# Kernel tuning notes

Hardware: AMD Instinct MI355X
Metric: run time of the kernel (lower is better)

The kernel has to match this reference:

```python
import jax, jax.numpy as jnp
import numpy as np

D_HEAD = 128
H_Q = 16
H_K = 4
D_MODEL = 2048
B = 2
T = 2048


def setup_inputs() -> dict:
    key = jax.random.key(0)
    k1, k2, k3, k4, k5 = jax.random.split(key, 5)
    s = 0.02
    return {
        "x": jax.random.normal(k1, (B, T, D_MODEL), dtype=jnp.float32),
        "wq": jax.random.normal(k2, (D_HEAD * H_Q, D_MODEL), dtype=jnp.float32) * s,
        "wk": jax.random.normal(k3, (D_HEAD * H_K, D_MODEL), dtype=jnp.float32) * s,
        "wv": jax.random.normal(k4, (D_HEAD * H_K, D_MODEL), dtype=jnp.float32) * s,
        "wo": jax.random.normal(k5, (D_MODEL, D_HEAD * H_Q), dtype=jnp.float32) * s,
    }


def reference(x, wq, wk, wv, wo):
    Bs, Ts, _ = x.shape
    g = H_Q // H_K  # query groups per kv head
    # projections (torch Linear: y = x @ W^T)
    Q = (x @ wq.T).reshape(Bs, Ts, H_Q, D_HEAD).transpose(0, 2, 1, 3)  # [B,hq,T,d]
    K = (x @ wk.T).reshape(Bs, Ts, H_K, D_HEAD).transpose(0, 2, 1, 3)  # [B,hk,T,d]
    V = (x @ wv.T).reshape(Bs, Ts, H_K, D_HEAD).transpose(0, 2, 1, 3)  # [B,hk,T,d]
    Qg = Q.reshape(Bs, g, H_K, Ts, D_HEAD)  # [B,g,hk,T,d]
    scale = D_HEAD ** -0.5
    attn = jnp.einsum("bghtd,bhsd->bghts", Qg, K) * scale  # [B,g,hk,T,T]
    causal = jnp.tril(jnp.ones((Ts, Ts), dtype=bool))
    attn = jnp.where(causal, attn, -jnp.inf)
    attn = jax.nn.softmax(attn, axis=-1)
    out = jnp.einsum("bghts,bhsd->bghtd", attn, V)  # [B,g,hk,T,d]
    out = out.reshape(Bs, H_Q, Ts, D_HEAD).transpose(0, 2, 1, 3).reshape(Bs, Ts, H_Q * D_HEAD)
    return out @ wo.T
```

## Files before the change

kernel.cpp:

```cpp
#include <hip/hip_runtime.h>
#include <hip/hip_bf16.h>
#include <stdint.h>

#define DMODEL 2048
#define HQ 16
#define HKV 4
#define DH 128
#define SEQT 2048
#define BATCH 2

typedef __bf16 bf16x8 __attribute__((ext_vector_type(8)));
typedef float f32x4 __attribute__((ext_vector_type(4)));
typedef float f32x16 __attribute__((ext_vector_type(16)));
typedef unsigned short u16x4 __attribute__((ext_vector_type(4)));
typedef unsigned short u16x8 __attribute__((ext_vector_type(8)));
typedef unsigned int u32x2 __attribute__((ext_vector_type(2)));

__device__ __forceinline__ unsigned short f2bf(float x) {
  __hip_bfloat16 h = __float2bfloat16(x);
  return __builtin_bit_cast(unsigned short, h);
}
__device__ __forceinline__ unsigned int cvtpk(float a, float b) {
  unsigned int r;
  asm("v_cvt_pk_bf16_f32 %0, %1, %2" : "=v"(r) : "v"(a), "v"(b));
  return r;
}

__device__ __forceinline__ void gload_lds16(const void* g, void* lds) {
  __builtin_amdgcn_global_load_lds(
      (const __attribute__((address_space(1))) void*)(uintptr_t)g,
      (__attribute__((address_space(3))) void*)(uint32_t)(uintptr_t)lds,
      16, 0, 0);
}

__global__ __launch_bounds__(256) void cast_all_kernel(
    const float* __restrict__ x, const float* __restrict__ wq,
    const float* __restrict__ wk, const float* __restrict__ wv,
    const float* __restrict__ wo,
    unsigned short* __restrict__ xb, unsigned short* __restrict__ wqb,
    unsigned short* __restrict__ wkb, unsigned short* __restrict__ wvb,
    unsigned short* __restrict__ wob) {
  int i = blockIdx.x * 256 + threadIdx.x;
  const float* in; unsigned short* out; int off; float s = 1.0f;
  if (i < 1048576)      { in = x;  out = xb;  off = i; }
  else if (i < 1572864) { in = wq; out = wqb; off = i - 1048576; s = 0.1275174473f; }
  else if (i < 1703936) { in = wk; out = wkb; off = i - 1572864; }
  else if (i < 1835008) { in = wv; out = wvb; off = i - 1703936; }
  else                  { in = wo; out = wob; off = i - 1835008; }
  const float4* p = reinterpret_cast<const float4*>(in) + (size_t)off * 2;
  float4 a = p[0], b = p[1];
  u16x8 o;
  o[0] = f2bf(a.x * s); o[1] = f2bf(a.y * s); o[2] = f2bf(a.z * s); o[3] = f2bf(a.w * s);
  o[4] = f2bf(b.x * s); o[5] = f2bf(b.y * s); o[6] = f2bf(b.z * s); o[7] = f2bf(b.w * s);
  *(reinterpret_cast<u16x8*>(out) + off) = o;
}

template <bool OUT_BF16>
__device__ __forceinline__ void gemm_body(
    unsigned short* As, unsigned short* Bs,
    const unsigned short* __restrict__ A, const unsigned short* __restrict__ B,
    void* __restrict__ Cv, int N, int K, int row0, int col0) {
  const int tid = threadIdx.x;
  const int wave = tid >> 6, lane = tid & 63;
  const int wr = (wave >> 1) * 64, wc = (wave & 1) * 64;
  const int l15 = lane & 15, l4 = lane >> 4;
  const int srow = wave * 32 + (lane >> 2);
  const int scol = (lane & 3) * 8;

  f32x4 acc[4][4] = {};

  for (int k0 = 0; k0 < K; k0 += 64) {
#pragma unroll
    for (int h = 0; h < 2; ++h) {
      const unsigned short* gA = A + (size_t)(row0 + srow) * K + k0 + h * 32 + scol;
      gload_lds16(gA, (char*)As + h * 8192 + wave * 2048);
      gload_lds16(gA + (size_t)16 * K, (char*)As + h * 8192 + wave * 2048 + 1024);
      const unsigned short* gB = B + (size_t)(col0 + srow) * K + k0 + h * 32 + scol;
      gload_lds16(gB, (char*)Bs + h * 8192 + wave * 2048);
      gload_lds16(gB + (size_t)16 * K, (char*)Bs + h * 8192 + wave * 2048 + 1024);
    }
    __syncthreads();

    bf16x8 af[2][4], bfr[2][4];
#pragma unroll
    for (int h = 0; h < 2; ++h)
#pragma unroll
      for (int i = 0; i < 4; ++i) {
        af[h][i]  = *reinterpret_cast<const bf16x8*>(&As[h * 4096 + (wr + i * 16 + l15) * 32 + l4 * 8]);
        bfr[h][i] = *reinterpret_cast<const bf16x8*>(&Bs[h * 4096 + (wc + i * 16 + l15) * 32 + l4 * 8]);
      }
#pragma unroll
    for (int h = 0; h < 2; ++h)
#pragma unroll
      for (int i = 0; i < 4; ++i)
#pragma unroll
        for (int j = 0; j < 4; ++j)
          acc[i][j] = __builtin_amdgcn_mfma_f32_16x16x32_bf16(af[h][i], bfr[h][j], acc[i][j], 0, 0, 0);
    __syncthreads();
  }

#pragma unroll
  for (int i = 0; i < 4; ++i) {
    const int rrow = row0 + wr + i * 16 + l4 * 4;
#pragma unroll
    for (int j = 0; j < 4; ++j) {
      const int ccol = col0 + wc + j * 16 + l15;
#pragma unroll
      for (int r = 0; r < 4; ++r) {
        const size_t idx = (size_t)(rrow + r) * N + ccol;
        if constexpr (OUT_BF16)
          ((unsigned short*)Cv)[idx] = f2bf(acc[i][j][r]);
        else
          ((float*)Cv)[idx] = acc[i][j][r];
      }
    }
  }
}

__global__ __launch_bounds__(256) void gemm_qkv(
    const unsigned short* __restrict__ xb, const unsigned short* __restrict__ wqb,
    const unsigned short* __restrict__ wkb, const unsigned short* __restrict__ wvb,
    unsigned short* __restrict__ Qb, unsigned short* __restrict__ Kb,
    unsigned short* __restrict__ VTb) {
  __shared__ alignas(16) unsigned short As[2][128 * 32];
  __shared__ alignas(16) unsigned short Bs[2][128 * 32];
  const int bid = blockIdx.x;
  if (bid < 512) {
    gemm_body<true>(&As[0][0], &Bs[0][0], xb, wqb, Qb, 2048, DMODEL,
                    (bid >> 4) * 128, (bid & 15) * 128);
  } else if (bid < 640) {
    const int r = bid - 512;
    gemm_body<true>(&As[0][0], &Bs[0][0], xb, wkb, Kb, 512, DMODEL,
                    (r >> 2) * 128, (r & 3) * 128);
  } else {
    const int r = bid - 640;
    const int tz = r & 1, ty = (r >> 1) & 15, tx = r >> 5;
    gemm_body<true>(&As[0][0], &Bs[0][0], wvb,
                    xb + (size_t)tz * SEQT * DMODEL,
                    VTb + (size_t)tz * 512 * SEQT, SEQT, DMODEL,
                    tx * 128, ty * 128);
  }
}

template <bool OUT_BF16>
__global__ __launch_bounds__(256) void gemm_bt(
    const unsigned short* __restrict__ A, const unsigned short* __restrict__ B,
    void* __restrict__ Cv, int N, int K) {
  __shared__ alignas(16) unsigned short As[2][128 * 32];
  __shared__ alignas(16) unsigned short Bs[2][128 * 32];
  gemm_body<OUT_BF16>(&As[0][0], &Bs[0][0], A, B, Cv, N, K,
                      blockIdx.x * 128, blockIdx.y * 128);
}

__global__ __launch_bounds__(256, 2) void attn_kernel(
    const unsigned short* __restrict__ Q, const unsigned short* __restrict__ Kc,
    const unsigned short* __restrict__ VT, unsigned short* __restrict__ AO) {
  __shared__ alignas(16) unsigned short Ks[2][16 * 512];
  __shared__ alignas(16) unsigned short Vs[2][16 * 512];

  const int tid = threadIdx.x;
  const int wave = tid >> 6, lane = tid & 63;
  const int bid = blockIdx.x;
  const int round = bid >> 8, pairslot = bid & 255;
  const int bhk = pairslot & 7;
  const int jp = pairslot >> 3;
  const int j = round ? jp : 63 - jp;
  const int b = bhk >> 2, hk = bhk & 3;
  const int h = hk + wave * 4;
  const int q0 = j * 32;
  const int jt = j >> 1;
  const int lq = lane & 31, hi = lane >> 5;

  const size_t qrow = (size_t)(b * SEQT + q0 + lq);
  const unsigned short* qp = Q + qrow * (HQ * DH) + h * DH + hi * 8;
  bf16x8 qf[8];
#pragma unroll
  for (int dc = 0; dc < 8; ++dc)
    qf[dc] = *reinterpret_cast<const bf16x8*>(qp + dc * 16);

  f32x16 acc[4] = {};
  float mrun = -INFINITY, lrun = 0.f;

  const unsigned short* kbase = Kc + (size_t)b * SEQT * (HKV * DH) + hk * DH;
  const unsigned short* vtb = VT + ((size_t)b * (HKV * DH) + hk * DH) * SEQT;

  auto STAGE = [&](int buf, int kvb2) {
#pragma unroll
    for (int i = 0; i < 4; ++i) {
      const int f = i * 4 + wave;
      const int sub = f >> 3, dc = f & 7;
      const unsigned short* g = kbase + (size_t)(kvb2 + sub * 32 + lq) * (HKV * DH) + dc * 16 + hi * 8;
      gload_lds16(g, (char*)Ks[buf] + f * 1024);
    }
#pragma unroll
    for (int i = 0; i < 4; ++i) {
      const int f = i * 4 + wave;
      const int dt = f >> 2, ks = f & 3;
      const unsigned short* g = vtb + (size_t)(dt * 32 + lq) * SEQT + kvb2 + ks * 16 + hi * 8;
      gload_lds16(g, (char*)Vs[buf] + f * 1024);
    }
  };

  STAGE(0, 0);
  __syncthreads();
  int cur = 0;

  for (int t = 0; t <= jt; ++t) {
    const int kvb = t * 64;
    if (t < jt) STAGE(cur ^ 1, kvb + 64);
    const bool s1v = (kvb + 32 <= q0);
    const bool d0 = (kvb == q0), d1 = (kvb + 32 == q0);
    const char* ksb = (const char*)Ks[cur];
    const char* vsb = (const char*)Vs[cur];

    f32x16 stA = {}, stB = {}, stA1 = {}, stB1 = {};
    __builtin_amdgcn_s_setprio(1);
#pragma unroll
    for (int dc = 0; dc < 4; ++dc) {
      bf16x8 kf = *reinterpret_cast<const bf16x8*>(ksb + dc * 1024 + lane * 16);
      stA = __builtin_amdgcn_mfma_f32_32x32x16_bf16(kf, qf[dc], stA, 0, 0, 0);
    }
#pragma unroll
    for (int dc = 4; dc < 8; ++dc) {
      bf16x8 kf = *reinterpret_cast<const bf16x8*>(ksb + dc * 1024 + lane * 16);
      stB = __builtin_amdgcn_mfma_f32_32x32x16_bf16(kf, qf[dc], stB, 0, 0, 0);
    }
    if (s1v) {
#pragma unroll
      for (int dc = 0; dc < 4; ++dc) {
        bf16x8 kf = *reinterpret_cast<const bf16x8*>(ksb + (8 + dc) * 1024 + lane * 16);
        stA1 = __builtin_amdgcn_mfma_f32_32x32x16_bf16(kf, qf[dc], stA1, 0, 0, 0);
      }
#pragma unroll
      for (int dc = 4; dc < 8; ++dc) {
        bf16x8 kf = *reinterpret_cast<const bf16x8*>(ksb + (8 + dc) * 1024 + lane * 16);
        stB1 = __builtin_amdgcn_mfma_f32_32x32x16_bf16(kf, qf[dc], stB1, 0, 0, 0);
      }
    }
    __builtin_amdgcn_s_setprio(0);

    float p0[16], p1[16];
#pragma unroll
    for (int r = 0; r < 16; ++r) p0[r] = stA[r] + stB[r];
    if (d0) {
#pragma unroll
      for (int r = 0; r < 16; ++r) {
        const int srw = (r & 3) + 8 * (r >> 2) + 4 * hi;
        if (srw > lq) p0[r] = -INFINITY;
      }
    }
    float m0, m1 = -INFINITY;
    {
      float a = fmaxf(fmaxf(p0[0], p0[1]), fmaxf(p0[2], p0[3]));
      float bm = fmaxf(fmaxf(p0[4], p0[5]), fmaxf(p0[6], p0[7]));
      float c = fmaxf(fmaxf(p0[8], p0[9]), fmaxf(p0[10], p0[11]));
      float dm = fmaxf(fmaxf(p0[12], p0[13]), fmaxf(p0[14], p0[15]));
      m0 = fmaxf(fmaxf(a, bm), fmaxf(c, dm));
    }
    if (s1v) {
#pragma unroll
      for (int r = 0; r < 16; ++r) p1[r] = stA1[r] + stB1[r];
      if (d1) {
#pragma unroll
        for (int r = 0; r < 16; ++r) {
          const int srw = (r & 3) + 8 * (r >> 2) + 4 * hi;
          if (srw > lq) p1[r] = -INFINITY;
        }
      }
      float a = fmaxf(fmaxf(p1[0], p1[1]), fmaxf(p1[2], p1[3]));
      float bm = fmaxf(fmaxf(p1[4], p1[5]), fmaxf(p1[6], p1[7]));
      float c = fmaxf(fmaxf(p1[8], p1[9]), fmaxf(p1[10], p1[11]));
      float dm = fmaxf(fmaxf(p1[12], p1[13]), fmaxf(p1[14], p1[15]));
      m1 = fmaxf(fmaxf(a, bm), fmaxf(c, dm));
    }
    float tmax = fmaxf(m0, m1);
    tmax = fmaxf(tmax, __shfl_xor(tmax, 32));
    if (!__all(tmax <= mrun)) {
      const float mnew = fmaxf(mrun, tmax);
      const float fsc = __builtin_amdgcn_exp2f(mrun - mnew);
      lrun *= fsc;
#pragma unroll
      for (int dt = 0; dt < 4; ++dt)
#pragma unroll
        for (int r = 0; r < 16; ++r) acc[dt][r] *= fsc;
      mrun = mnew;
    }
    float psum;
    {
#pragma unroll
      for (int r = 0; r < 16; ++r) p0[r] = __builtin_amdgcn_exp2f(p0[r] - mrun);
      float t0 = (p0[0] + p0[1]) + (p0[2] + p0[3]);
      float t1 = (p0[4] + p0[5]) + (p0[6] + p0[7]);
      float t2 = (p0[8] + p0[9]) + (p0[10] + p0[11]);
      float t3 = (p0[12] + p0[13]) + (p0[14] + p0[15]);
      psum = (t0 + t1) + (t2 + t3);
    }
    if (s1v) {
#pragma unroll
      for (int r = 0; r < 16; ++r) p1[r] = __builtin_amdgcn_exp2f(p1[r] - mrun);
      float t0 = (p1[0] + p1[1]) + (p1[2] + p1[3]);
      float t1 = (p1[4] + p1[5]) + (p1[6] + p1[7]);
      float t2 = (p1[8] + p1[9]) + (p1[10] + p1[11]);
      float t3 = (p1[12] + p1[13]) + (p1[14] + p1[15]);
      psum += (t0 + t1) + (t2 + t3);
    }

    union { unsigned int u[4]; bf16x8 v; } pf0, pf1, pf2, pf3;
    {
      unsigned int x0 = cvtpk(p0[0], p0[1]),  x1 = cvtpk(p0[2], p0[3]);
      unsigned int x2 = cvtpk(p0[4], p0[5]),  x3 = cvtpk(p0[6], p0[7]);
      unsigned int x4 = cvtpk(p0[8], p0[9]),  x5 = cvtpk(p0[10], p0[11]);
      unsigned int x6 = cvtpk(p0[12], p0[13]), x7 = cvtpk(p0[14], p0[15]);
      unsigned int x0s = __shfl_xor(x0, 32), x1s = __shfl_xor(x1, 32);
      unsigned int x2s = __shfl_xor(x2, 32), x3s = __shfl_xor(x3, 32);
      unsigned int x4s = __shfl_xor(x4, 32), x5s = __shfl_xor(x5, 32);
      unsigned int x6s = __shfl_xor(x6, 32), x7s = __shfl_xor(x7, 32);
      pf0.u[0] = hi ? x2s : x0;  pf0.u[1] = hi ? x3s : x1;
      pf0.u[2] = hi ? x2  : x0s; pf0.u[3] = hi ? x3  : x1s;
      pf1.u[0] = hi ? x6s : x4;  pf1.u[1] = hi ? x7s : x5;
      pf1.u[2] = hi ? x6  : x4s; pf1.u[3] = hi ? x7  : x5s;
    }
    if (s1v) {
      unsigned int x0 = cvtpk(p1[0], p1[1]),  x1 = cvtpk(p1[2], p1[3]);
      unsigned int x2 = cvtpk(p1[4], p1[5]),  x3 = cvtpk(p1[6], p1[7]);
      unsigned int x4 = cvtpk(p1[8], p1[9]),  x5 = cvtpk(p1[10], p1[11]);
      unsigned int x6 = cvtpk(p1[12], p1[13]), x7 = cvtpk(p1[14], p1[15]);
      unsigned int x0s = __shfl_xor(x0, 32), x1s = __shfl_xor(x1, 32);
      unsigned int x2s = __shfl_xor(x2, 32), x3s = __shfl_xor(x3, 32);
      unsigned int x4s = __shfl_xor(x4, 32), x5s = __shfl_xor(x5, 32);
      unsigned int x6s = __shfl_xor(x6, 32), x7s = __shfl_xor(x7, 32);
      pf2.u[0] = hi ? x2s : x0;  pf2.u[1] = hi ? x3s : x1;
      pf2.u[2] = hi ? x2  : x0s; pf2.u[3] = hi ? x3  : x1s;
      pf3.u[0] = hi ? x6s : x4;  pf3.u[1] = hi ? x7s : x5;
      pf3.u[2] = hi ? x6  : x4s; pf3.u[3] = hi ? x7  : x5s;
    }
    psum += __shfl_xor(psum, 32);
    lrun += psum;

    __builtin_amdgcn_s_setprio(1);
#pragma unroll
    for (int dt = 0; dt < 4; ++dt) {
      bf16x8 v0 = *reinterpret_cast<const bf16x8*>(vsb + (dt * 4 + 0) * 1024 + lane * 16);
      bf16x8 v1 = *reinterpret_cast<const bf16x8*>(vsb + (dt * 4 + 1) * 1024 + lane * 16);
      acc[dt] = __builtin_amdgcn_mfma_f32_32x32x16_bf16(v0, pf0.v, acc[dt], 0, 0, 0);
      acc[dt] = __builtin_amdgcn_mfma_f32_32x32x16_bf16(v1, pf1.v, acc[dt], 0, 0, 0);
    }
    if (s1v) {
#pragma unroll
      for (int dt = 0; dt < 4; ++dt) {
        bf16x8 v2 = *reinterpret_cast<const bf16x8*>(vsb + (dt * 4 + 2) * 1024 + lane * 16);
        bf16x8 v3 = *reinterpret_cast<const bf16x8*>(vsb + (dt * 4 + 3) * 1024 + lane * 16);
        acc[dt] = __builtin_amdgcn_mfma_f32_32x32x16_bf16(v2, pf2.v, acc[dt], 0, 0, 0);
        acc[dt] = __builtin_amdgcn_mfma_f32_32x32x16_bf16(v3, pf3.v, acc[dt], 0, 0, 0);
      }
    }
    __builtin_amdgcn_s_setprio(0);
    __syncthreads();
    cur ^= 1;
  }

  const float inv = 1.f / lrun;
  unsigned short* op = AO + qrow * (HQ * DH) + h * DH;
#pragma unroll
  for (int dt = 0; dt < 4; ++dt) {
#pragma unroll
    for (int g2 = 0; g2 < 4; ++g2) {
      u32x2 w;
      w[0] = cvtpk(acc[dt][g2 * 4 + 0] * inv, acc[dt][g2 * 4 + 1] * inv);
      w[1] = cvtpk(acc[dt][g2 * 4 + 2] * inv, acc[dt][g2 * 4 + 3] * inv);
      *reinterpret_cast<u32x2*>(op + dt * 32 + g2 * 8 + 4 * hi) = w;
    }
  }
}

extern "C" void kernel_launch(void* const* d_in, const int* in_sizes, int n_in,
                              void* d_out, int out_size, void* d_ws, size_t ws_size,
                              hipStream_t stream) {
  const float* x  = (const float*)d_in[0];
  const float* wq = (const float*)d_in[1];
  const float* wk = (const float*)d_in[2];
  const float* wv = (const float*)d_in[3];
  const float* wo = (const float*)d_in[4];
  float* out = (float*)d_out;

  const size_t N_X  = (size_t)BATCH * SEQT * DMODEL;
  const size_t N_WQ = (size_t)HQ * DH * DMODEL;
  const size_t N_WK = (size_t)HKV * DH * DMODEL;
  const size_t N_Q  = (size_t)BATCH * SEQT * HQ * DH;
  const size_t N_K  = (size_t)BATCH * SEQT * HKV * DH;

  unsigned short* xb  = (unsigned short*)d_ws;
  unsigned short* wqb = xb  + N_X;
  unsigned short* wkb = wqb + N_WQ;
  unsigned short* wvb = wkb + N_WK;
  unsigned short* wob = wvb + N_WK;
  unsigned short* Qb  = wob + N_WQ;
  unsigned short* Kb  = Qb  + N_Q;
  unsigned short* VTb = Kb  + N_K;
  unsigned short* AOb = VTb + N_K;

  cast_all_kernel<<<dim3(9216), dim3(256), 0, stream>>>(
      x, wq, wk, wv, wo, xb, wqb, wkb, wvb, wob);

  gemm_qkv<<<dim3(768), 256, 0, stream>>>(xb, wqb, wkb, wvb, Qb, Kb, VTb);
  attn_kernel<<<dim3(512, 1, 1), 256, 0, stream>>>(Qb, Kb, VTb, AOb);
  gemm_bt<false><<<dim3(32, 16, 1), 256, 0, stream>>>(AOb, wob, out, 2048, DMODEL);
}
```

Measured before the change: 191.0 us.

## Split attention KV range into two halves with separate merge kernel

Each attention block now processes only every other 32-wide KV tile (split-K over the KV sequence), which doubles the grid and halves the LDS stage. Occupancy is raised to 4 blocks per CU. Partial unnormalized outputs and running max/sum values are written to workspace that reuses the cast-input region, and a new merge kernel combines the two halves with rescaling before the output projection. This adds an extra kernel launch, extra global traffic for the partials, and bf16 rounding of the unnormalized partial outputs.

```diff
diff --git a/kernel.cpp b/kernel.cpp
--- a/kernel.cpp
+++ b/kernel.cpp
@@ -8,6 +8,7 @@
 #define DH 128
 #define SEQT 2048
 #define BATCH 2
+#define NQTOT 8388608ull
 
 typedef __bf16 bf16x8 __attribute__((ext_vector_type(8)));
 typedef float f32x4 __attribute__((ext_vector_type(4)));
@@ -19,6 +20,10 @@
 __device__ __forceinline__ unsigned short f2bf(float x) {
   __hip_bfloat16 h = __float2bfloat16(x);
   return __builtin_bit_cast(unsigned short, h);
+}
+__device__ __forceinline__ float bf2f(unsigned short u) {
+  unsigned int x = ((unsigned int)u) << 16;
+  return __builtin_bit_cast(float, x);
 }
 __device__ __forceinline__ unsigned int cvtpk(float a, float b) {
   unsigned int r;
@@ -152,23 +157,24 @@
                       blockIdx.x * 128, blockIdx.y * 128);
 }
 
-__global__ __launch_bounds__(256, 2) void attn_kernel(
+__global__ __launch_bounds__(256, 4) void attn_kernel(
     const unsigned short* __restrict__ Q, const unsigned short* __restrict__ Kc,
-    const unsigned short* __restrict__ VT, unsigned short* __restrict__ AO) {
-  __shared__ alignas(16) unsigned short Ks[2][16 * 512];
-  __shared__ alignas(16) unsigned short Vs[2][16 * 512];
+    const unsigned short* __restrict__ VT, unsigned short* __restrict__ Op,
+    float* __restrict__ ml) {
+  __shared__ alignas(16) unsigned short Ks[2][8 * 512];
+  __shared__ alignas(16) unsigned short Vs[2][8 * 512];
 
   const int tid = threadIdx.x;
   const int wave = tid >> 6, lane = tid & 63;
   const int bid = blockIdx.x;
-  const int round = bid >> 8, pairslot = bid & 255;
-  const int bhk = pairslot & 7;
-  const int jp = pairslot >> 3;
-  const int j = round ? jp : 63 - jp;
+  const int bhk = bid & 7;
+  const int slot = bid >> 3;
+  const int half = slot & 1;
+  const int jj = slot >> 1;
+  const int j = (jj & 1) ? (jj >> 1) : (63 - (jj >> 1));
   const int b = bhk >> 2, hk = bhk & 3;
   const int h = hk + wave * 4;
   const int q0 = j * 32;
-  const int jt = j >> 1;
   const int lq = lane & 31, hi = lane >> 5;
 
   const size_t qrow = (size_t)(b * SEQT + q0 + lq);
@@ -184,36 +190,33 @@
   const unsigned short* kbase = Kc + (size_t)b * SEQT * (HKV * DH) + hk * DH;
   const unsigned short* vtb = VT + ((size_t)b * (HKV * DH) + hk * DH) * SEQT;
 
-  auto STAGE = [&](int buf, int kvb2) {
-#pragma unroll
-    for (int i = 0; i < 4; ++i) {
+  auto STAGE = [&](int buf, int kvb) {
+#pragma unroll
+    for (int i = 0; i < 2; ++i) {
       const int f = i * 4 + wave;
-      const int sub = f >> 3, dc = f & 7;
-      const unsigned short* g = kbase + (size_t)(kvb2 + sub * 32 + lq) * (HKV * DH) + dc * 16 + hi * 8;
+      const unsigned short* g = kbase + (size_t)(kvb + lq) * (HKV * DH) + f * 16 + hi * 8;
       gload_lds16(g, (char*)Ks[buf] + f * 1024);
     }
 #pragma unroll
-    for (int i = 0; i < 4; ++i) {
+    for (int i = 0; i < 2; ++i) {
       const int f = i * 4 + wave;
-      const int dt = f >> 2, ks = f & 3;
-      const unsigned short* g = vtb + (size_t)(dt * 32 + lq) * SEQT + kvb2 + ks * 16 + hi * 8;
+      const int dt = f >> 1, ks = f & 1;
+      const unsigned short* g = vtb + (size_t)(dt * 32 + lq) * SEQT + kvb + ks * 16 + hi * 8;
       gload_lds16(g, (char*)Vs[buf] + f * 1024);
     }
   };
 
-  STAGE(0, 0);
+  int t = half;
+  if (t <= j) STAGE(0, t * 32);
   __syncthreads();
   int cur = 0;
 
-  for (int t = 0; t <= jt; ++t) {
-    const int kvb = t * 64;
-    if (t < jt) STAGE(cur ^ 1, kvb + 64);
-    const bool s1v = (kvb + 32 <= q0);
-    const bool d0 = (kvb == q0), d1 = (kvb + 32 == q0);
+  for (; t <= j; t += 2) {
+    if (t + 2 <= j) STAGE(cur ^ 1, (t + 2) * 32);
     const char* ksb = (const char*)Ks[cur];
     const char* vsb = (const char*)Vs[cur];
 
-    f32x16 stA = {}, stB = {}, stA1 = {}, stB1 = {};
+    f32x16 stA = {}, stB = {};
     __builtin_amdgcn_s_setprio(1);
 #pragma unroll
     for (int dc = 0; dc < 4; ++dc) {
@@ -225,31 +228,19 @@
       bf16x8 kf = *reinterpret_cast<const bf16x8*>(ksb + dc * 1024 + lane * 16);
       stB = __builtin_amdgcn_mfma_f32_32x32x16_bf16(kf, qf[dc], stB, 0, 0, 0);
     }
-    if (s1v) {
-#pragma unroll
-      for (int dc = 0; dc < 4; ++dc) {
-        bf16x8 kf = *reinterpret_cast<const bf16x8*>(ksb + (8 + dc) * 1024 + lane * 16);
-        stA1 = __builtin_amdgcn_mfma_f32_32x32x16_bf16(kf, qf[dc], stA1, 0, 0, 0);
-      }
-#pragma unroll
-      for (int dc = 4; dc < 8; ++dc) {
-        bf16x8 kf = *reinterpret_cast<const bf16x8*>(ksb + (8 + dc) * 1024 + lane * 16);
-        stB1 = __builtin_amdgcn_mfma_f32_32x32x16_bf16(kf, qf[dc], stB1, 0, 0, 0);
-      }
-    }
     __builtin_amdgcn_s_setprio(0);
 
-    float p0[16], p1[16];
+    float p0[16];
 #pragma unroll
     for (int r = 0; r < 16; ++r) p0[r] = stA[r] + stB[r];
-    if (d0) {
+    if (t == j) {
 #pragma unroll
       for (int r = 0; r < 16; ++r) {
         const int srw = (r & 3) + 8 * (r >> 2) + 4 * hi;
         if (srw > lq) p0[r] = -INFINITY;
       }
     }
-    float m0, m1 = -INFINITY;
+    float m0;
     {
       float a = fmaxf(fmaxf(p0[0], p0[1]), fmaxf(p0[2], p0[3]));
       float bm = fmaxf(fmaxf(p0[4], p0[5]), fmaxf(p0[6], p0[7]));
@@ -257,24 +248,7 @@
       float dm = fmaxf(fmaxf(p0[12], p0[13]), fmaxf(p0[14], p0[15]));
       m0 = fmaxf(fmaxf(a, bm), fmaxf(c, dm));
     }
-    if (s1v) {
-#pragma unroll
-      for (int r = 0; r < 16; ++r) p1[r] = stA1[r] + stB1[r];
-      if (d1) {
-#pragma unroll
-        for (int r = 0; r < 16; ++r) {
-          const int srw = (r & 3) + 8 * (r >> 2) + 4 * hi;
-          if (srw > lq) p1[r] = -INFINITY;
-        }
-      }
-      float a = fmaxf(fmaxf(p1[0], p1[1]), fmaxf(p1[2], p1[3]));
-      float bm = fmaxf(fmaxf(p1[4], p1[5]), fmaxf(p1[6], p1[7]));
-      float c = fmaxf(fmaxf(p1[8], p1[9]), fmaxf(p1[10], p1[11]));
-      float dm = fmaxf(fmaxf(p1[12], p1[13]), fmaxf(p1[14], p1[15]));
-      m1 = fmaxf(fmaxf(a, bm), fmaxf(c, dm));
-    }
-    float tmax = fmaxf(m0, m1);
-    tmax = fmaxf(tmax, __shfl_xor(tmax, 32));
+    float tmax = fmaxf(m0, __shfl_xor(m0, 32));
     if (!__all(tmax <= mrun)) {
       const float mnew = fmaxf(mrun, tmax);
       const float fsc = __builtin_amdgcn_exp2f(mrun - mnew);
@@ -295,17 +269,8 @@
       float t3 = (p0[12] + p0[13]) + (p0[14] + p0[15]);
       psum = (t0 + t1) + (t2 + t3);
     }
-    if (s1v) {
-#pragma unroll
-      for (int r = 0; r < 16; ++r) p1[r] = __builtin_amdgcn_exp2f(p1[r] - mrun);
-      float t0 = (p1[0] + p1[1]) + (p1[2] + p1[3]);
-      float t1 = (p1[4] + p1[5]) + (p1[6] + p1[7]);
-      float t2 = (p1[8] + p1[9]) + (p1[10] + p1[11]);
-      float t3 = (p1[12] + p1[13]) + (p1[14] + p1[15]);
-      psum += (t0 + t1) + (t2 + t3);
-    }
-
-    union { unsigned int u[4]; bf16x8 v; } pf0, pf1, pf2, pf3;
+
+    union { unsigned int u[4]; bf16x8 v; } pf0, pf1;
     {
       unsigned int x0 = cvtpk(p0[0], p0[1]),  x1 = cvtpk(p0[2], p0[3]);
       unsigned int x2 = cvtpk(p0[4], p0[5]),  x3 = cvtpk(p0[6], p0[7]);
@@ -320,57 +285,66 @@
       pf1.u[0] = hi ? x6s : x4;  pf1.u[1] = hi ? x7s : x5;
       pf1.u[2] = hi ? x6  : x4s; pf1.u[3] = hi ? x7  : x5s;
     }
-    if (s1v) {
-      unsigned int x0 = cvtpk(p1[0], p1[1]),  x1 = cvtpk(p1[2], p1[3]);
-      unsigned int x2 = cvtpk(p1[4], p1[5]),  x3 = cvtpk(p1[6], p1[7]);
-      unsigned int x4 = cvtpk(p1[8], p1[9]),  x5 = cvtpk(p1[10], p1[11]);
-      unsigned int x6 = cvtpk(p1[12], p1[13]), x7 = cvtpk(p1[14], p1[15]);
-      unsigned int x0s = __shfl_xor(x0, 32), x1s = __shfl_xor(x1, 32);
-      unsigned int x2s = __shfl_xor(x2, 32), x3s = __shfl_xor(x3, 32);
-      unsigned int x4s = __shfl_xor(x4, 32), x5s = __shfl_xor(x5, 32);
-      unsigned int x6s = __shfl_xor(x6, 32), x7s = __shfl_xor(x7, 32);
-      pf2.u[0] = hi ? x2s : x0;  pf2.u[1] = hi ? x3s : x1;
-      pf2.u[2] = hi ? x2  : x0s; pf2.u[3] = hi ? x3  : x1s;
-      pf3.u[0] = hi ? x6s : x4;  pf3.u[1] = hi ? x7s : x5;
-      pf3.u[2] = hi ? x6  : x4s; pf3.u[3] = hi ? x7  : x5s;
-    }
     psum += __shfl_xor(psum, 32);
     lrun += psum;
 
     __builtin_amdgcn_s_setprio(1);
 #pragma unroll
     for (int dt = 0; dt < 4; ++dt) {
-      bf16x8 v0 = *reinterpret_cast<const bf16x8*>(vsb + (dt * 4 + 0) * 1024 + lane * 16);
-      bf16x8 v1 = *reinterpret_cast<const bf16x8*>(vsb + (dt * 4 + 1) * 1024 + lane * 16);
+      bf16x8 v0 = *reinterpret_cast<const bf16x8*>(vsb + (dt * 2 + 0) * 1024 + lane * 16);
+      bf16x8 v1 = *reinterpret_cast<const bf16x8*>(vsb + (dt * 2 + 1) * 1024 + lane * 16);
       acc[dt] = __builtin_amdgcn_mfma_f32_32x32x16_bf16(v0, pf0.v, acc[dt], 0, 0, 0);
       acc[dt] = __builtin_amdgcn_mfma_f32_32x32x16_bf16(v1, pf1.v, acc[dt], 0, 0, 0);
-    }
-    if (s1v) {
-#pragma unroll
-      for (int dt = 0; dt < 4; ++dt) {
-        bf16x8 v2 = *reinterpret_cast<const bf16x8*>(vsb + (dt * 4 + 2) * 1024 + lane * 16);
-        bf16x8 v3 = *reinterpret_cast<const bf16x8*>(vsb + (dt * 4 + 3) * 1024 + lane * 16);
-        acc[dt] = __builtin_amdgcn_mfma_f32_32x32x16_bf16(v2, pf2.v, acc[dt], 0, 0, 0);
-        acc[dt] = __builtin_amdgcn_mfma_f32_32x32x16_bf16(v3, pf3.v, acc[dt], 0, 0, 0);
-      }
     }
     __builtin_amdgcn_s_setprio(0);
     __syncthreads();
     cur ^= 1;
   }
 
-  const float inv = 1.f / lrun;
-  unsigned short* op = AO + qrow * (HQ * DH) + h * DH;
+  unsigned short* op = Op + (size_t)half * NQTOT + qrow * (HQ * DH) + h * DH;
 #pragma unroll
   for (int dt = 0; dt < 4; ++dt) {
 #pragma unroll
     for (int g2 = 0; g2 < 4; ++g2) {
       u32x2 w;
-      w[0] = cvtpk(acc[dt][g2 * 4 + 0] * inv, acc[dt][g2 * 4 + 1] * inv);
-      w[1] = cvtpk(acc[dt][g2 * 4 + 2] * inv, acc[dt][g2 * 4 + 3] * inv);
+      w[0] = cvtpk(acc[dt][g2 * 4 + 0], acc[dt][g2 * 4 + 1]);
+      w[1] = cvtpk(acc[dt][g2 * 4 + 2], acc[dt][g2 * 4 + 3]);
       *reinterpret_cast<u32x2*>(op + dt * 32 + g2 * 8 + 4 * hi) = w;
     }
   }
+  if (hi == 0) {
+    const size_t mi = ((size_t)half * 65536 + qrow * 16 + h) * 2;
+    ml[mi] = mrun;
+    ml[mi + 1] = lrun;
+  }
+}
+
+__global__ __launch_bounds__(256) void merge_kernel(
+    const unsigned short* __restrict__ Op, const float* __restrict__ ml,
+    unsigned short* __restrict__ AO) {
+  const int gid = blockIdx.x * 256 + threadIdx.x;
+  const int rh = gid >> 4;
+  const int dp = (gid & 15) * 8;
+  const size_t obase = (size_t)rh * 128 + dp;
+
+  const float m1 = ml[(size_t)rh * 2], l1 = ml[(size_t)rh * 2 + 1];
+  const float m2 = ml[((size_t)65536 + rh) * 2], l2 = ml[((size_t)65536 + rh) * 2 + 1];
+  const float m = fmaxf(m1, m2);
+  float a1 = __builtin_amdgcn_exp2f(m1 - m);
+  float a2 = __builtin_amdgcn_exp2f(m2 - m);
+  const float inv = 1.f / (a1 * l1 + a2 * l2);
+  a1 *= inv; a2 *= inv;
+
+  u16x8 o1 = *reinterpret_cast<const u16x8*>(Op + obase);
+  u16x8 o2 = *reinterpret_cast<const u16x8*>(Op + NQTOT + obase);
+  union { unsigned int u[4]; u16x8 v; } w;
+#pragma unroll
+  for (int k = 0; k < 8; k += 2) {
+    float fa = a1 * bf2f(o1[k])     + a2 * bf2f(o2[k]);
+    float fb = a1 * bf2f(o1[k + 1]) + a2 * bf2f(o2[k + 1]);
+    w.u[k >> 1] = cvtpk(fa, fb);
+  }
+  *reinterpret_cast<u16x8*>(AO + obase) = w.v;
 }
 
 extern "C" void kernel_launch(void* const* d_in, const int* in_sizes, int n_in,
@@ -389,20 +363,23 @@
   const size_t N_Q  = (size_t)BATCH * SEQT * HQ * DH;
   const size_t N_K  = (size_t)BATCH * SEQT * HKV * DH;
 
-  unsigned short* xb  = (unsigned short*)d_ws;
-  unsigned short* wqb = xb  + N_X;
-  unsigned short* wkb = wqb + N_WQ;
-  unsigned short* wvb = wkb + N_WK;
-  unsigned short* wob = wvb + N_WK;
+  unsigned short* wob = (unsigned short*)d_ws;
   unsigned short* Qb  = wob + N_WQ;
   unsigned short* Kb  = Qb  + N_Q;
   unsigned short* VTb = Kb  + N_K;
   unsigned short* AOb = VTb + N_K;
+  unsigned short* xb  = AOb + N_Q;
+  unsigned short* wqb = xb  + N_X;
+  unsigned short* wkb = wqb + N_WQ;
+  unsigned short* wvb = wkb + N_WK;
+  unsigned short* Op  = xb;
+  float* ml           = (float*)(Op + 2 * N_Q);
 
   cast_all_kernel<<<dim3(9216), dim3(256), 0, stream>>>(
       x, wq, wk, wv, wo, xb, wqb, wkb, wvb, wob);
 
   gemm_qkv<<<dim3(768), 256, 0, stream>>>(xb, wqb, wkb, wvb, Qb, Kb, VTb);
-  attn_kernel<<<dim3(512, 1, 1), 256, 0, stream>>>(Qb, Kb, VTb, AOb);
+  attn_kernel<<<dim3(1024, 1, 1), 256, 0, stream>>>(Qb, Kb, VTb, Op, ml);
+  merge_kernel<<<dim3(4096), 256, 0, stream>>>(Op, ml, AOb);
   gemm_bt<false><<<dim3(32, 16, 1), 256, 0, stream>>>(AOb, wob, out, 2048, DMODEL);
 }
```

Result: slower. 272.8 us (+42.8%).

## Software-pipeline attention: overlap QK^T of next tile with softmax/PV of previous

Applied to the files above, without the earlier changes.

Restructures the attention loop so each iteration computes the QK^T MFMAs for the current KV tile and then runs the softmax and PV accumulation for the previous tile. V gets a third LDS buffer so the previous tile's V stays resident while the next one is staged. The goal is to interleave matrix-core work with the exp/max/shuffle VALU work. In exchange it adds register pressure from carrying p0/p1 across iterations and extra LDS, which could hurt occupancy at two blocks per CU. The final tile's softmax and PV run in an epilogue after the loop, and FINISH is always called with S1=true inside the loop, which relies on every non-final tile being full.

```diff
diff --git a/kernel.cpp b/kernel.cpp
--- a/kernel.cpp
+++ b/kernel.cpp
@@ -156,7 +156,7 @@
     const unsigned short* __restrict__ Q, const unsigned short* __restrict__ Kc,
     const unsigned short* __restrict__ VT, unsigned short* __restrict__ AO) {
   __shared__ alignas(16) unsigned short Ks[2][16 * 512];
-  __shared__ alignas(16) unsigned short Vs[2][16 * 512];
+  __shared__ alignas(16) unsigned short Vs[3][16 * 512];
 
   const int tid = threadIdx.x;
   const int wave = tid >> 6, lane = tid & 63;
@@ -180,11 +180,12 @@
 
   f32x16 acc[4] = {};
   float mrun = -INFINITY, lrun = 0.f;
+  float p0[16], p1[16];
 
   const unsigned short* kbase = Kc + (size_t)b * SEQT * (HKV * DH) + hk * DH;
   const unsigned short* vtb = VT + ((size_t)b * (HKV * DH) + hk * DH) * SEQT;
 
-  auto STAGE = [&](int buf, int kvb2) {
+  auto STAGE_K = [&](int buf, int kvb2) {
 #pragma unroll
     for (int i = 0; i < 4; ++i) {
       const int f = i * 4 + wave;
@@ -192,63 +193,18 @@
       const unsigned short* g = kbase + (size_t)(kvb2 + sub * 32 + lq) * (HKV * DH) + dc * 16 + hi * 8;
       gload_lds16(g, (char*)Ks[buf] + f * 1024);
     }
+  };
+  auto STAGE_V = [&](int slot, int kvb2) {
 #pragma unroll
     for (int i = 0; i < 4; ++i) {
       const int f = i * 4 + wave;
       const int dt = f >> 2, ks = f & 3;
       const unsigned short* g = vtb + (size_t)(dt * 32 + lq) * SEQT + kvb2 + ks * 16 + hi * 8;
-      gload_lds16(g, (char*)Vs[buf] + f * 1024);
+      gload_lds16(g, (char*)Vs[slot] + f * 1024);
     }
   };
 
-  STAGE(0, 0);
-  __syncthreads();
-  int cur = 0;
-
-  for (int t = 0; t <= jt; ++t) {
-    const int kvb = t * 64;
-    if (t < jt) STAGE(cur ^ 1, kvb + 64);
-    const bool s1v = (kvb + 32 <= q0);
-    const bool d0 = (kvb == q0), d1 = (kvb + 32 == q0);
-    const char* ksb = (const char*)Ks[cur];
-    const char* vsb = (const char*)Vs[cur];
-
-    f32x16 stA = {}, stB = {}, stA1 = {}, stB1 = {};
-    __builtin_amdgcn_s_setprio(1);
-#pragma unroll
-    for (int dc = 0; dc < 4; ++dc) {
-      bf16x8 kf = *reinterpret_cast<const bf16x8*>(ksb + dc * 1024 + lane * 16);
-      stA = __builtin_amdgcn_mfma_f32_32x32x16_bf16(kf, qf[dc], stA, 0, 0, 0);
-    }
-#pragma unroll
-    for (int dc = 4; dc < 8; ++dc) {
-      bf16x8 kf = *reinterpret_cast<const bf16x8*>(ksb + dc * 1024 + lane * 16);
-      stB = __builtin_amdgcn_mfma_f32_32x32x16_bf16(kf, qf[dc], stB, 0, 0, 0);
-    }
-    if (s1v) {
-#pragma unroll
-      for (int dc = 0; dc < 4; ++dc) {
-        bf16x8 kf = *reinterpret_cast<const bf16x8*>(ksb + (8 + dc) * 1024 + lane * 16);
-        stA1 = __builtin_amdgcn_mfma_f32_32x32x16_bf16(kf, qf[dc], stA1, 0, 0, 0);
-      }
-#pragma unroll
-      for (int dc = 4; dc < 8; ++dc) {
-        bf16x8 kf = *reinterpret_cast<const bf16x8*>(ksb + (8 + dc) * 1024 + lane * 16);
-        stB1 = __builtin_amdgcn_mfma_f32_32x32x16_bf16(kf, qf[dc], stB1, 0, 0, 0);
-      }
-    }
-    __builtin_amdgcn_s_setprio(0);
-
-    float p0[16], p1[16];
-#pragma unroll
-    for (int r = 0; r < 16; ++r) p0[r] = stA[r] + stB[r];
-    if (d0) {
-#pragma unroll
-      for (int r = 0; r < 16; ++r) {
-        const int srw = (r & 3) + 8 * (r >> 2) + 4 * hi;
-        if (srw > lq) p0[r] = -INFINITY;
-      }
-    }
+  auto FINISH = [&](bool S1, const char* vsb) {
     float m0, m1 = -INFINITY;
     {
       float a = fmaxf(fmaxf(p0[0], p0[1]), fmaxf(p0[2], p0[3]));
@@ -257,16 +213,7 @@
       float dm = fmaxf(fmaxf(p0[12], p0[13]), fmaxf(p0[14], p0[15]));
       m0 = fmaxf(fmaxf(a, bm), fmaxf(c, dm));
     }
-    if (s1v) {
-#pragma unroll
-      for (int r = 0; r < 16; ++r) p1[r] = stA1[r] + stB1[r];
-      if (d1) {
-#pragma unroll
-        for (int r = 0; r < 16; ++r) {
-          const int srw = (r & 3) + 8 * (r >> 2) + 4 * hi;
-          if (srw > lq) p1[r] = -INFINITY;
-        }
-      }
+    if (S1) {
       float a = fmaxf(fmaxf(p1[0], p1[1]), fmaxf(p1[2], p1[3]));
       float bm = fmaxf(fmaxf(p1[4], p1[5]), fmaxf(p1[6], p1[7]));
       float c = fmaxf(fmaxf(p1[8], p1[9]), fmaxf(p1[10], p1[11]));
@@ -295,7 +242,7 @@
       float t3 = (p0[12] + p0[13]) + (p0[14] + p0[15]);
       psum = (t0 + t1) + (t2 + t3);
     }
-    if (s1v) {
+    if (S1) {
 #pragma unroll
       for (int r = 0; r < 16; ++r) p1[r] = __builtin_amdgcn_exp2f(p1[r] - mrun);
       float t0 = (p1[0] + p1[1]) + (p1[2] + p1[3]);
@@ -320,7 +267,7 @@
       pf1.u[0] = hi ? x6s : x4;  pf1.u[1] = hi ? x7s : x5;
       pf1.u[2] = hi ? x6  : x4s; pf1.u[3] = hi ? x7  : x5s;
     }
-    if (s1v) {
+    if (S1) {
       unsigned int x0 = cvtpk(p1[0], p1[1]),  x1 = cvtpk(p1[2], p1[3]);
       unsigned int x2 = cvtpk(p1[4], p1[5]),  x3 = cvtpk(p1[6], p1[7]);
       unsigned int x4 = cvtpk(p1[8], p1[9]),  x5 = cvtpk(p1[10], p1[11]);
@@ -345,7 +292,7 @@
       acc[dt] = __builtin_amdgcn_mfma_f32_32x32x16_bf16(v0, pf0.v, acc[dt], 0, 0, 0);
       acc[dt] = __builtin_amdgcn_mfma_f32_32x32x16_bf16(v1, pf1.v, acc[dt], 0, 0, 0);
     }
-    if (s1v) {
+    if (S1) {
 #pragma unroll
       for (int dt = 0; dt < 4; ++dt) {
         bf16x8 v2 = *reinterpret_cast<const bf16x8*>(vsb + (dt * 4 + 2) * 1024 + lane * 16);
@@ -355,9 +302,75 @@
       }
     }
     __builtin_amdgcn_s_setprio(0);
+  };
+
+  STAGE_K(0, 0);
+  STAGE_V(0, 0);
+  __syncthreads();
+  int kc = 0, vt = 0, vp = 2, vn = 1;
+
+  for (int t = 0; t <= jt; ++t) {
+    const int kvb = t * 64;
+    if (t < jt) { STAGE_K(kc ^ 1, kvb + 64); STAGE_V(vn, kvb + 64); }
+
+    const bool s1v = (kvb + 32 <= q0);
+    const bool d0 = (kvb == q0), d1 = (kvb + 32 == q0);
+    const char* ksb = (const char*)Ks[kc];
+
+    f32x16 stA = {}, stB = {}, stA1 = {}, stB1 = {};
+    __builtin_amdgcn_s_setprio(1);
+#pragma unroll
+    for (int dc = 0; dc < 4; ++dc) {
+      bf16x8 kf = *reinterpret_cast<const bf16x8*>(ksb + dc * 1024 + lane * 16);
+      stA = __builtin_amdgcn_mfma_f32_32x32x16_bf16(kf, qf[dc], stA, 0, 0, 0);
+    }
+#pragma unroll
+    for (int dc = 4; dc < 8; ++dc) {
+      bf16x8 kf = *reinterpret_cast<const bf16x8*>(ksb + dc * 1024 + lane * 16);
+      stB = __builtin_amdgcn_mfma_f32_32x32x16_bf16(kf, qf[dc], stB, 0, 0, 0);
+    }
+    if (s1v) {
+#pragma unroll
+      for (int dc = 0; dc < 4; ++dc) {
+        bf16x8 kf = *reinterpret_cast<const bf16x8*>(ksb + (8 + dc) * 1024 + lane * 16);
+        stA1 = __builtin_amdgcn_mfma_f32_32x32x16_bf16(kf, qf[dc], stA1, 0, 0, 0);
+      }
+#pragma unroll
+      for (int dc = 4; dc < 8; ++dc) {
+        bf16x8 kf = *reinterpret_cast<const bf16x8*>(ksb + (8 + dc) * 1024 + lane * 16);
+        stB1 = __builtin_amdgcn_mfma_f32_32x32x16_bf16(kf, qf[dc], stB1, 0, 0, 0);
+      }
+    }
+    __builtin_amdgcn_s_setprio(0);
+
+    if (t > 0) FINISH(true, (const char*)Vs[vp]);
+
+#pragma unroll
+    for (int r = 0; r < 16; ++r) p0[r] = stA[r] + stB[r];
+    if (d0) {
+#pragma unroll
+      for (int r = 0; r < 16; ++r) {
+        const int srw = (r & 3) + 8 * (r >> 2) + 4 * hi;
+        if (srw > lq) p0[r] = -INFINITY;
+      }
+    }
+    if (s1v) {
+#pragma unroll
+      for (int r = 0; r < 16; ++r) p1[r] = stA1[r] + stB1[r];
+      if (d1) {
+#pragma unroll
+        for (int r = 0; r < 16; ++r) {
+          const int srw = (r & 3) + 8 * (r >> 2) + 4 * hi;
+          if (srw > lq) p1[r] = -INFINITY;
+        }
+      }
+    }
+
     __syncthreads();
-    cur ^= 1;
+    const int ovp = vp; vp = vt; vt = vn; vn = ovp; kc ^= 1;
   }
+
+  FINISH(jt * 64 + 32 <= q0, (const char*)Vs[vp]);
 
   const float inv = 1.f / lrun;
   unsigned short* op = AO + qrow * (HQ * DH) + h * DH;
```

New measurement: 195.9 us. 1.03x slower.

## Double-buffer GEMM LDS tiles to overlap global loads with MFMA

Applied to the files above, without the earlier changes.

The GEMM main loop now stages K-chunks of 32 into two alternating LDS buffers, issuing the load for the next chunk before computing on the current one. This lets the global-to-LDS copies overlap with MFMA work, where before each step loaded 64 of K and then waited. The trade-off is half the work per iteration and one barrier per 32-wide step, so there are twice as many syncs. The new loop also relies on a single barrier per iteration to cover both the load and the reuse of the buffer.

```diff
diff --git a/kernel.cpp b/kernel.cpp
--- a/kernel.cpp
+++ b/kernel.cpp
@@ -69,34 +69,38 @@
 
   f32x4 acc[4][4] = {};
 
-  for (int k0 = 0; k0 < K; k0 += 64) {
-#pragma unroll
-    for (int h = 0; h < 2; ++h) {
-      const unsigned short* gA = A + (size_t)(row0 + srow) * K + k0 + h * 32 + scol;
-      gload_lds16(gA, (char*)As + h * 8192 + wave * 2048);
-      gload_lds16(gA + (size_t)16 * K, (char*)As + h * 8192 + wave * 2048 + 1024);
-      const unsigned short* gB = B + (size_t)(col0 + srow) * K + k0 + h * 32 + scol;
-      gload_lds16(gB, (char*)Bs + h * 8192 + wave * 2048);
-      gload_lds16(gB + (size_t)16 * K, (char*)Bs + h * 8192 + wave * 2048 + 1024);
-    }
+  auto STAGE = [&](int buf, int k0) {
+    const unsigned short* gA = A + (size_t)(row0 + srow) * K + k0 + scol;
+    gload_lds16(gA, (char*)As + buf * 8192 + wave * 2048);
+    gload_lds16(gA + (size_t)16 * K, (char*)As + buf * 8192 + wave * 2048 + 1024);
+    const unsigned short* gB = B + (size_t)(col0 + srow) * K + k0 + scol;
+    gload_lds16(gB, (char*)Bs + buf * 8192 + wave * 2048);
+    gload_lds16(gB + (size_t)16 * K, (char*)Bs + buf * 8192 + wave * 2048 + 1024);
+  };
+
+  STAGE(0, 0);
+  __syncthreads();
+  int cur = 0;
+
+  for (int k0 = 0; k0 < K; k0 += 32) {
+    if (k0 + 32 < K) STAGE(cur ^ 1, k0 + 32);
+
+    const unsigned short* as = As + cur * 4096;
+    const unsigned short* bs = Bs + cur * 4096;
+    bf16x8 af[4], bfr[4];
+#pragma unroll
+    for (int i = 0; i < 4; ++i) {
+      af[i]  = *reinterpret_cast<const bf16x8*>(&as[(wr + i * 16 + l15) * 32 + l4 * 8]);
+      bfr[i] = *reinterpret_cast<const bf16x8*>(&bs[(wc + i * 16 + l15) * 32 + l4 * 8]);
+    }
+#pragma unroll
+    for (int i = 0; i < 4; ++i)
+#pragma unroll
+      for (int j = 0; j < 4; ++j)
+        acc[i][j] = __builtin_amdgcn_mfma_f32_16x16x32_bf16(af[i], bfr[j], acc[i][j], 0, 0, 0);
+
     __syncthreads();
-
-    bf16x8 af[2][4], bfr[2][4];
-#pragma unroll
-    for (int h = 0; h < 2; ++h)
-#pragma unroll
-      for (int i = 0; i < 4; ++i) {
-        af[h][i]  = *reinterpret_cast<const bf16x8*>(&As[h * 4096 + (wr + i * 16 + l15) * 32 + l4 * 8]);
-        bfr[h][i] = *reinterpret_cast<const bf16x8*>(&Bs[h * 4096 + (wc + i * 16 + l15) * 32 + l4 * 8]);
-      }
-#pragma unroll
-    for (int h = 0; h < 2; ++h)
-#pragma unroll
-      for (int i = 0; i < 4; ++i)
-#pragma unroll
-        for (int j = 0; j < 4; ++j)
-          acc[i][j] = __builtin_amdgcn_mfma_f32_16x16x32_bf16(af[h][i], bfr[h][j], acc[i][j], 0, 0, 0);
-    __syncthreads();
+    cur ^= 1;
   }
 
 #pragma unroll
```

Result: no change. 192.0 us (+0.5%).
